# Optimization experiments

Hardware: AMD Instinct MI355X
Metric: run time of the kernel (lower is better)

Reference implementation:

```python
import jax, jax.numpy as jnp
import numpy as np

HEADS = 4
KNN_K = 20
BN_EPS = 1e-5


def conv1x1(w, b, x):
    # 1x1 Conv1d: w [out, in], x [B, in, N] -> [B, out, N]
    return jnp.einsum('oc,bcn->bon', w, x) + b[None, :, None]


def setup_inputs() -> dict:
    key = jax.random.key(0)
    B, C, N = 2, 128, 2048
    ks = jax.random.split(key, 16)
    W = lambda k, o, i: jax.random.normal(k, (o, i), jnp.float32) * 0.05
    V = lambda k, o: jax.random.normal(k, (o,), jnp.float32) * 0.05
    return {
        'desc1': jax.random.normal(ks[0], (B, C, N, 1), jnp.float32),
        'wq': W(ks[1], C, C), 'bq': V(ks[2], C),
        'wk': W(ks[3], C, C), 'bk': V(ks[4], C),
        'wv': W(ks[5], C, C), 'bv': V(ks[6], C),
        'wm': W(ks[7], C, C), 'bm': V(ks[8], C),
        'w1': W(ks[9], 2 * C, 2 * C), 'b1': V(ks[10], 2 * C),
        'gamma': jnp.ones((2 * C,), jnp.float32),
        'beta': jnp.zeros((2 * C,), jnp.float32),
        'w2': W(ks[11], C, 2 * C), 'b2': V(ks[12], C),
    }


def reference(desc1, wq, bq, wk, bk, wv, bv, wm, bm, w1, b1, gamma, beta, w2, b2):
    x = desc1[..., 0]                      # [B, C, N]
    B, C, N = x.shape
    D = C // HEADS

    q = conv1x1(wq, bq, x).reshape(B, HEADS, D, N)
    k = conv1x1(wk, bk, x).reshape(B, HEADS, D, N)
    v = conv1x1(wv, bv, x).reshape(B, HEADS, D, N)

    # kNN on raw descriptors: pd = -||xi||^2 + 2 xi.xj - ||xj||^2 (larger = closer)
    xx = jnp.sum(x * x, axis=1)            # [B, N]
    pd = 2.0 * jnp.einsum('bcn,bcm->bnm', x, x) - xx[:, :, None] - xx[:, None, :]
    idx = jax.lax.top_k(pd, KNN_K)[1]      # [B, N, K]

    # scatter ones at kNN indices, then keep only mutual neighbors
    bI = jnp.arange(B)[:, None, None]
    nI = jnp.arange(N)[None, :, None]
    mask = jnp.zeros((B, N, N), x.dtype).at[bI, nI, idx].set(1.0)
    mask = mask * mask.transpose(0, 2, 1)  # [B, N, N]

    score = jnp.einsum('bhdn,bhdm->bhnm', q, k) / (D ** 0.5)
    m = mask[:, None]                      # broadcast over heads
    score = score * m + (-1e9) * (1.0 - m)
    score = jax.nn.softmax(score, axis=-1)

    av = jnp.einsum('bhnm,bhdm->bhdn', score, v).reshape(B, C, N)
    av = conv1x1(wm, bm, av)

    h = conv1x1(w1, b1, jnp.concatenate([x, av], axis=1))  # [B, 2C, N]
    mu = jnp.mean(h, axis=(0, 2), keepdims=True)
    var = jnp.var(h, axis=(0, 2), keepdims=True)           # biased, matches torch BN
    h = (h - mu) / jnp.sqrt(var + BN_EPS) * gamma[None, :, None] + beta[None, :, None]
    h = jax.nn.relu(h)

    out = x + conv1x1(w2, b2, h)
    return out[..., None]                  # [B, C, N, 1]
```

## Files before the change

### kernel.cpp

```cpp
#include <hip/hip_runtime.h>
#include <math.h>

#define NPT 2048
#define KNN 20

typedef const float* fp;
typedef __attribute__((ext_vector_type(4))) float f32x4;
typedef __attribute__((ext_vector_type(8))) short s16x8;

__device__ __forceinline__ ushort f2bf_rne(float v) {
    unsigned u = __float_as_uint(v);
    unsigned r = u + 0x7FFFu + ((u >> 16) & 1u);
    return (ushort)(r >> 16);
}
__device__ __forceinline__ float bfbits2f(ushort h) {
    return __uint_as_float(((unsigned)h) << 16);
}
__device__ __forceinline__ s16x8 ldfrag(const ushort* p) {
    union { uint4 u; s16x8 s; } cv;
    cv.u = *reinterpret_cast<const uint4*>(p);
    return cv.s;
}
__device__ __forceinline__ void f8_hilo(const float* row, s16x8* hi, s16x8* lo) {
    float4 f0 = *reinterpret_cast<const float4*>(row);
    float4 f1 = *reinterpret_cast<const float4*>(row + 4);
    float f[8] = {f0.x, f0.y, f0.z, f0.w, f1.x, f1.y, f1.z, f1.w};
    union { ushort u[8]; s16x8 s; } H, L;
    #pragma unroll
    for (int j = 0; j < 8; j++) {
        ushort h = f2bf_rne(f[j]);
        H.u[j] = h;
        L.u[j] = f2bf_rne(f[j] - bfbits2f(h));
    }
    *hi = H.s; *lo = L.s;
}

__global__ __launch_bounds__(256) void prep_all(
    fp xbf, fp wq, fp wk, fp wv, fp wm, fp w1, fp w2, fp bm, fp b1,
    float* xx, ushort* xhiF, ushort* xloF,
    ushort* wqFhi, ushort* wqFlo, ushort* wkFhi, ushort* wkFlo,
    ushort* wvFhi, ushort* wvFlo,
    ushort* wcFhi, ushort* wcFlo, ushort* w2Fhi, ushort* w2Flo,
    float* b1p, float* stats) {
    int t = threadIdx.x;
    if (blockIdx.x < 256) {
        __shared__ float xs[16][129];
        __shared__ float xpart[16][17];
        int p0 = blockIdx.x * 16;
        int b = p0 >> 11, n0 = p0 & 2047;
        fp xb = xbf + (size_t)b * 128 * NPT;
        {
            int c = t >> 1, half = t & 1;
            float4 f0 = *reinterpret_cast<const float4*>(xb + (size_t)c * NPT + n0 + half * 8);
            float4 f1 = *reinterpret_cast<const float4*>(xb + (size_t)c * NPT + n0 + half * 8 + 4);
            xs[half * 8 + 0][c] = f0.x; xs[half * 8 + 1][c] = f0.y;
            xs[half * 8 + 2][c] = f0.z; xs[half * 8 + 3][c] = f0.w;
            xs[half * 8 + 4][c] = f1.x; xs[half * 8 + 5][c] = f1.y;
            xs[half * 8 + 6][c] = f1.z; xs[half * 8 + 7][c] = f1.w;
        }
        __syncthreads();
        int p = t & 15, g = t >> 4, c0 = g * 8;
        float f[8];
        #pragma unroll
        for (int j = 0; j < 8; j++) f[j] = xs[p][c0 + j];
        float ps = 0.f;
        #pragma unroll
        for (int j = 0; j < 8; j++) ps += f[j] * f[j];
        xpart[p][g] = ps;
        union { ushort u[8]; uint4 q; } H, L;
        #pragma unroll
        for (int j = 0; j < 8; j++) {
            ushort hi = f2bf_rne(f[j]);
            H.u[j] = hi;
            L.u[j] = f2bf_rne(f[j] - bfbits2f(hi));
        }
        size_t off = ((size_t)blockIdx.x * 4 + (c0 >> 5)) * 512
                   + (size_t)(((((c0 >> 3) & 3) * 16) + p) * 8);
        *reinterpret_cast<uint4*>(xhiF + off) = H.q;
        *reinterpret_cast<uint4*>(xloF + off) = L.q;
        __syncthreads();
        if (t < 16) {
            float s = 0.f;
            #pragma unroll
            for (int gg = 0; gg < 16; gg++) s += xpart[t][gg];
            xx[p0 + t] = s;
        }
        return;
    }
    int wid = (blockIdx.x - 256) * 256 + t;
    if (wid < 49152) {
        int which = wid >> 14, e = wid & 16383;
        int lane = (e >> 3) & 63, j = e & 7, kk = (e >> 9) & 3, nt = e >> 11;
        int n = nt * 16 + (lane & 15);
        int k = kk * 32 + (lane >> 4) * 8 + j;
        fp src = which == 0 ? wq : which == 1 ? wk : wv;
        float v = src[n * 128 + k];
        ushort hi = f2bf_rne(v);
        (which == 0 ? wqFhi : which == 1 ? wkFhi : wvFhi)[e] = hi;
        (which == 0 ? wqFlo : which == 1 ? wkFlo : wvFlo)[e] = f2bf_rne(v - bfbits2f(hi));
    } else if (wid < 114688) {
        int e = wid - 49152;
        int j = e & 7, lane = (e >> 3) & 63, kk = (e >> 9) & 7, nt = e >> 12;
        int n = nt * 16 + (lane & 15);
        int k = kk * 32 + (lane >> 4) * 8 + j;
        float v;
        if (k < 128) {
            v = w1[n * 256 + k];
        } else {
            int c = k - 128;
            float s = 0.f;
            for (int i = 0; i < 128; i += 4) {
                float4 wr = *reinterpret_cast<const float4*>(w1 + n * 256 + 128 + i);
                s += wr.x * wm[(i + 0) * 128 + c];
                s += wr.y * wm[(i + 1) * 128 + c];
                s += wr.z * wm[(i + 2) * 128 + c];
                s += wr.w * wm[(i + 3) * 128 + c];
            }
            v = s;
        }
        ushort hi = f2bf_rne(v);
        wcFhi[e] = hi;
        wcFlo[e] = f2bf_rne(v - bfbits2f(hi));
    } else if (wid < 147456) {
        int e = wid - 114688;
        int j = e & 7, lane = (e >> 3) & 63, kk = (e >> 9) & 7, nt = e >> 12;
        int n = nt * 16 + (lane & 15);
        int k = kk * 32 + (lane >> 4) * 8 + j;
        float v = w2[n * 256 + k];
        ushort hi = f2bf_rne(v);
        w2Fhi[e] = hi;
        w2Flo[e] = f2bf_rne(v - bfbits2f(hi));
    } else if (wid < 147712) {
        int o = wid - 147456;
        float s = b1[o];
        for (int i = 0; i < 128; i++)
            s += w1[o * 256 + 128 + i] * bm[i];
        b1p[o] = s;
    } else {
        stats[wid - 147712] = 0.0f;
    }
}

#define MERGE(off) { float ov = __shfl_xor(bv, off); int oi = __shfl_xor(bi, off); \
                     if (ov > bv || (ov == bv && oi < bi)) { bv = ov; bi = oi; } }

#define KEYPAIR(C0, D0, D1) { \
    int ct0 = slab * 128 + w * 8 + C0; \
    int ct1 = ct0 + 1; \
    f32x4 a0 = (f32x4){0.f, 0.f, 0.f, 0.f}; \
    f32x4 a1 = (f32x4){0.f, 0.f, 0.f, 0.f}; \
    _Pragma("unroll 2") \
    for (int kk = 0; kk < 4; kk++) { \
        s16x8 ah = ldfrag(Ahi[kk] + lane * 8); \
        s16x8 al = ldfrag(Alo[kk] + lane * 8); \
        s16x8 b0h = ldfrag(xhiF + ((size_t)(ct0 * 4 + kk)) * 512 + lane * 8); \
        s16x8 b0l = ldfrag(xloF + ((size_t)(ct0 * 4 + kk)) * 512 + lane * 8); \
        s16x8 b1h = ldfrag(xhiF + ((size_t)(ct1 * 4 + kk)) * 512 + lane * 8); \
        s16x8 b1l = ldfrag(xloF + ((size_t)(ct1 * 4 + kk)) * 512 + lane * 8); \
        a0 = __builtin_amdgcn_mfma_f32_16x16x32_bf16(ah, b0h, a0, 0, 0, 0); \
        a1 = __builtin_amdgcn_mfma_f32_16x16x32_bf16(ah, b1h, a1, 0, 0, 0); \
        a0 = __builtin_amdgcn_mfma_f32_16x16x32_bf16(al, b0h, a0, 0, 0, 0); \
        a1 = __builtin_amdgcn_mfma_f32_16x16x32_bf16(al, b1h, a1, 0, 0, 0); \
        a0 = __builtin_amdgcn_mfma_f32_16x16x32_bf16(ah, b0l, a0, 0, 0, 0); \
        a1 = __builtin_amdgcn_mfma_f32_16x16x32_bf16(ah, b1l, a1, 0, 0, 0); \
    } \
    float xx0 = xx[slab * 2048 + (w * 8 + C0) * 16 + cl]; \
    float xx1 = xx[slab * 2048 + (w * 8 + C0 + 1) * 16 + cl]; \
    a0[0] = 2.0f * a0[0] - xx0; a0[1] = 2.0f * a0[1] - xx0; \
    a0[2] = 2.0f * a0[2] - xx0; a0[3] = 2.0f * a0[3] - xx0; \
    a1[0] = 2.0f * a1[0] - xx1; a1[1] = 2.0f * a1[1] - xx1; \
    a1[2] = 2.0f * a1[2] - xx1; a1[3] = 2.0f * a1[3] - xx1; \
    D0 = a0; D1 = a1; \
}

__global__ __launch_bounds__(1024, 4) void gemm_key_topk(
    const ushort* xhiF, const ushort* xloF, const float* xx,
    const ushort* wqFhi, const ushort* wqFlo,
    const ushort* wkFhi, const ushort* wkFlo,
    const ushort* wvFhi, const ushort* wvFlo,
    fp bq, fp bk, fp bv_, float* qT, float* kT, float* vT,
    int* idxbuf, float* scratch) {
    __shared__ ushort Ahi[4][512];
    __shared__ ushort Alo[4][512];
    __shared__ float chm[16][64];
    __shared__ float sv[16][256];
    __shared__ int   si[16][256];
    __shared__ float Trow[16];
    __shared__ int   rowcnt[16];
    __shared__ int   ovfAll;
    int tt = threadIdx.x, w = tt >> 6, lane = tt & 63;
    int rt = blockIdx.x;
    int slab = rt >> 7, rtl = rt & 127;
    int cl = lane & 15, quad = lane >> 4;

    if (tt < 16) rowcnt[tt] = 0;

    if (tt < 512) {
        int which = tt >> 8, kk = (tt >> 6) & 3, ln = tt & 63;
        const ushort* src = (which ? xloF : xhiF)
                          + ((size_t)(rt * 4 + kk)) * 512 + ln * 8;
        uint4 v = *reinterpret_cast<const uint4*>(src);
        *reinterpret_cast<uint4*>((which ? Alo[kk] : Ahi[kk]) + ln * 8) = v;
    }
    __syncthreads();

    if (w < 12) {
        f32x4 acc0 = (f32x4){0.f, 0.f, 0.f, 0.f};
        f32x4 acc1 = (f32x4){0.f, 0.f, 0.f, 0.f};
        int pair0 = w * 2, pair1 = w * 2 + 1;
        int mat0 = pair0 >> 3, nt0 = pair0 & 7;
        int mat1 = pair1 >> 3, nt1 = pair1 & 7;
        const ushort* w0hi = mat0 == 0 ? wqFhi : mat0 == 1 ? wkFhi : wvFhi;
        const ushort* w0lo = mat0 == 0 ? wqFlo : mat0 == 1 ? wkFlo : wvFlo;
        const ushort* w1hi = mat1 == 0 ? wqFhi : mat1 == 1 ? wkFhi : wvFhi;
        const ushort* w1lo = mat1 == 0 ? wqFlo : mat1 == 1 ? wkFlo : wvFlo;
        #pragma unroll 2
        for (int kk = 0; kk < 4; kk++) {
            s16x8 ah = ldfrag(Ahi[kk] + lane * 8);
            s16x8 al = ldfrag(Alo[kk] + lane * 8);
            s16x8 b0h = ldfrag(w0hi + ((size_t)(nt0 * 4 + kk)) * 512 + lane * 8);
            s16x8 b0l = ldfrag(w0lo + ((size_t)(nt0 * 4 + kk)) * 512 + lane * 8);
            s16x8 b1h = ldfrag(w1hi + ((size_t)(nt1 * 4 + kk)) * 512 + lane * 8);
            s16x8 b1l = ldfrag(w1lo + ((size_t)(nt1 * 4 + kk)) * 512 + lane * 8);
            acc0 = __builtin_amdgcn_mfma_f32_16x16x32_bf16(ah, b0h, acc0, 0, 0, 0);
            acc1 = __builtin_amdgcn_mfma_f32_16x16x32_bf16(ah, b1h, acc1, 0, 0, 0);
            acc0 = __builtin_amdgcn_mfma_f32_16x16x32_bf16(al, b0h, acc0, 0, 0, 0);
            acc1 = __builtin_amdgcn_mfma_f32_16x16x32_bf16(al, b1h, acc1, 0, 0, 0);
            acc0 = __builtin_amdgcn_mfma_f32_16x16x32_bf16(ah, b0l, acc0, 0, 0, 0);
            acc1 = __builtin_amdgcn_mfma_f32_16x16x32_bf16(ah, b1l, acc1, 0, 0, 0);
        }
        int p0 = rt * 16;
        {
            fp bias    = mat0 == 0 ? bq : mat0 == 1 ? bk : bv_;
            float* out = mat0 == 0 ? qT : mat0 == 1 ? kT : vT;
            int o = nt0 * 16 + cl;
            float bvv = bias[o];
            #pragma unroll
            for (int r = 0; r < 4; r++)
                out[(size_t)(p0 + quad * 4 + r) * 128 + o] = acc0[r] + bvv;
        }
        {
            fp bias    = mat1 == 0 ? bq : mat1 == 1 ? bk : bv_;
            float* out = mat1 == 0 ? qT : mat1 == 1 ? kT : vT;
            int o = nt1 * 16 + cl;
            float bvv = bias[o];
            #pragma unroll
            for (int r = 0; r < 4; r++)
                out[(size_t)(p0 + quad * 4 + r) * 128 + o] = acc1[r] + bvv;
        }
    }
    __builtin_amdgcn_sched_barrier(0);

    f32x4 key0, key1, key2, key3, key4, key5, key6, key7;
    KEYPAIR(0, key0, key1)
    __builtin_amdgcn_sched_barrier(0);
    KEYPAIR(2, key2, key3)
    __builtin_amdgcn_sched_barrier(0);
    KEYPAIR(4, key4, key5)
    __builtin_amdgcn_sched_barrier(0);
    KEYPAIR(6, key6, key7)
    __builtin_amdgcn_sched_barrier(0);

    {
        float m[4];
        #pragma unroll
        for (int r = 0; r < 4; r++) {
            float mm = fmaxf(fmaxf(fmaxf(key0[r], key1[r]), fmaxf(key2[r], key3[r])),
                             fmaxf(fmaxf(key4[r], key5[r]), fmaxf(key6[r], key7[r])));
            mm = fmaxf(mm, __shfl_xor(mm, 1));
            mm = fmaxf(mm, __shfl_xor(mm, 2));
            m[r] = mm;
        }
        if ((cl & 3) == 0) {
            #pragma unroll
            for (int r = 0; r < 4; r++)
                chm[quad * 4 + r][w * 4 + (cl >> 2)] = m[r];
        }
    }
    __syncthreads();

    {
        float bs = chm[w][lane];
        #pragma unroll
        for (int k = 2; k <= 64; k <<= 1) {
            #pragma unroll
            for (int j = k >> 1; j > 0; j >>= 1) {
                float o = __shfl_xor(bs, j);
                bool dirDesc = (lane & k) != 0;
                bool upper   = (lane & j) != 0;
                bs = (upper != dirDesc) ? fmaxf(bs, o) : fminf(bs, o);
            }
        }
        float T = __shfl(bs, 44);
        if (lane == 0) Trow[w] = T;
    }
    __syncthreads();

    #pragma unroll
    for (int r = 0; r < 4; r++) {
        int row = quad * 4 + r;
        float T = Trow[row];
        float vals[8] = {key0[r], key1[r], key2[r], key3[r],
                         key4[r], key5[r], key6[r], key7[r]};
        #pragma unroll
        for (int c = 0; c < 8; c++) {
            float v = vals[c];
            if (v >= T) {
                int pos = atomicAdd(&rowcnt[row], 1);
                if (pos < 256) {
                    sv[row][pos] = v;
                    si[row][pos] = (w * 8 + c) * 16 + cl;
                }
            }
        }
    }
    __syncthreads();
    if (tt == 0) {
        int o = 0;
        for (int i = 0; i < 16; i++) o |= (rowcnt[i] > 256) ? 1 : 0;
        ovfAll = o;
    }
    __syncthreads();
    int ovf = ovfAll;

    int S = rowcnt[w];
    int rowg = slab * 2048 + rtl * 16 + w;
    if (S <= 64) {
        float v; int idx;
        if (lane < S) { v = sv[w][lane]; idx = si[w][lane]; }
        else          { v = -3.4e38f;    idx = 0x7FFFFFFF; }
        #pragma unroll
        for (int k = 2; k <= 64; k <<= 1) {
            #pragma unroll
            for (int j = k >> 1; j > 0; j >>= 1) {
                float ov = __shfl_xor(v, j); int oi = __shfl_xor(idx, j);
                bool dirDesc = (lane & k) != 0;
                bool upper   = (lane & j) != 0;
                bool takeMax = (upper != dirDesc);
                bool amax = (v > ov) || (v == ov && idx < oi);
                if (takeMax != amax) { v = ov; idx = oi; }
            }
        }
        if (lane >= 44) idxbuf[(size_t)rowg * KNN + (63 - lane)] = idx;
    } else if (S <= 256) {
        float vl[4]; int il[4];
        #pragma unroll
        for (int s = 0; s < 4; s++) {
            int g = lane + s * 64;
            bool ok = g < S;
            vl[s] = ok ? sv[w][g] : -3.4e38f;
            il[s] = ok ? si[w][g] : 0x7FFFFFFF;
        }
        unsigned removed = 0u;
        for (int iter = 0; iter < KNN; iter++) {
            float bv = -3.4e38f; int bi = 0x7FFFFFFF;
            #pragma unroll
            for (int s = 0; s < 4; s++) {
                bool live = ((removed >> s) & 1u) == 0u;
                if (live && (vl[s] > bv || (vl[s] == bv && il[s] < bi))) {
                    bv = vl[s]; bi = il[s];
                }
            }
            MERGE(32) MERGE(16) MERGE(8) MERGE(4) MERGE(2) MERGE(1)
            if (lane == 0) idxbuf[(size_t)rowg * KNN + iter] = bi;
            #pragma unroll
            for (int s = 0; s < 4; s++)
                if (il[s] == bi) removed |= 1u << s;
        }
    }

    if (ovf) {
        #pragma unroll
        for (int r = 0; r < 4; r++) {
            float vals[8] = {key0[r], key1[r], key2[r], key3[r],
                             key4[r], key5[r], key6[r], key7[r]};
            #pragma unroll
            for (int c = 0; c < 8; c++)
                scratch[((size_t)rt * 16 + quad * 4 + r) * 2048
                        + (w * 8 + c) * 16 + cl] = vals[c];
        }
        __syncthreads();
        if (rowcnt[w] > 256) {
            const float* rowp = scratch + ((size_t)rt * 16 + w) * 2048;
            float rv[32];
            #pragma unroll
            for (int j = 0; j < 32; j++) rv[j] = rowp[j * 64 + lane];
            unsigned removed = 0u;
            for (int iter = 0; iter < KNN; iter++) {
                float bv = -3.4e38f; int bi = 0;
                #pragma unroll
                for (int sl = 0; sl < 32; sl++) {
                    bool live = ((removed >> sl) & 1u) == 0u;
                    if (live && rv[sl] > bv) { bv = rv[sl]; bi = sl * 64 + lane; }
                }
                MERGE(32) MERGE(16) MERGE(8) MERGE(4) MERGE(2) MERGE(1)
                if (lane == 0) idxbuf[(size_t)rowg * KNN + iter] = bi;
                if ((bi & 63) == lane) removed |= 1u << (bi >> 6);
            }
        }
    }
}

__global__ __launch_bounds__(256) void k3_attn(
    fp qT, fp kT, fp vT, const int* idxbuf, float* avT) {
    __shared__ float sbuf[2][KNN * 4];
    __shared__ int   mlist[2][KNN];
    __shared__ int   cnt_s[2];
    int tt = threadIdx.x;
    int half = tt >> 7, t = tt & 127;
    int p = blockIdx.x * 2 + half;
    int b = p >> 11, n = p & 2047;
    int bbase = b * NPT;
    int h = t >> 5;

    if ((tt >> 6) == half * 2) {
        int lane = tt & 63;
        bool fl = false; int m = 0;
        if (lane < KNN) {
            m = idxbuf[(size_t)p * KNN + lane] & 2047;
            const int4* mrow = reinterpret_cast<const int4*>(idxbuf + (size_t)(bbase + m) * KNN);
            int4 r0 = mrow[0], r1 = mrow[1], r2 = mrow[2], r3 = mrow[3], r4 = mrow[4];
            fl = (r0.x == n) || (r0.y == n) || (r0.z == n) || (r0.w == n)
              || (r1.x == n) || (r1.y == n) || (r1.z == n) || (r1.w == n)
              || (r2.x == n) || (r2.y == n) || (r2.z == n) || (r2.w == n)
              || (r3.x == n) || (r3.y == n) || (r3.z == n) || (r3.w == n)
              || (r4.x == n) || (r4.y == n) || (r4.z == n) || (r4.w == n);
        }
        unsigned long long mask = __ballot(fl);
        int pos = __popcll(mask & ((1ull << lane) - 1ull));
        if (fl) mlist[half][pos] = m;
        if (lane == 0) cnt_s[half] = (int)__popcll(mask);
    }
    __syncthreads();

    int cnt = cnt_s[half];
    float qv = qT[(size_t)p * 128 + t];
    int jj = 0;
    for (; jj + 1 < cnt; jj += 2) {
        int m0 = mlist[half][jj], m1 = mlist[half][jj + 1];
        float pr0 = qv * kT[(size_t)(bbase + m0) * 128 + t];
        float pr1 = qv * kT[(size_t)(bbase + m1) * 128 + t];
        pr0 += __shfl_xor(pr0, 16); pr1 += __shfl_xor(pr1, 16);
        pr0 += __shfl_xor(pr0, 8);  pr1 += __shfl_xor(pr1, 8);
        pr0 += __shfl_xor(pr0, 4);  pr1 += __shfl_xor(pr1, 4);
        pr0 += __shfl_xor(pr0, 2);  pr1 += __shfl_xor(pr1, 2);
        pr0 += __shfl_xor(pr0, 1);  pr1 += __shfl_xor(pr1, 1);
        if ((t & 31) == 0) {
            sbuf[half][jj * 4 + h]       = pr0 * 0.17677669529663687f;
            sbuf[half][(jj + 1) * 4 + h] = pr1 * 0.17677669529663687f;
        }
    }
    if (jj < cnt) {
        int m = mlist[half][jj];
        float prod = qv * kT[(size_t)(bbase + m) * 128 + t];
        prod += __shfl_xor(prod, 16);
        prod += __shfl_xor(prod, 8);
        prod += __shfl_xor(prod, 4);
        prod += __shfl_xor(prod, 2);
        prod += __shfl_xor(prod, 1);
        if ((t & 31) == 0) sbuf[half][jj * 4 + h] = prod * 0.17677669529663687f;
    }
    __syncthreads();

    float mx = -3.4e38f;
    for (int j = 0; j < cnt; j++) mx = fmaxf(mx, sbuf[half][j * 4 + h]);
    float den = 0.f, accv = 0.f;
    for (int j = 0; j < cnt; j++) {
        float ex = expf(sbuf[half][j * 4 + h] - mx);
        den += ex;
        accv += ex * vT[(size_t)(bbase + mlist[half][j]) * 128 + t];
    }
    float inv = (cnt > 0) ? (1.0f / den) : 0.0f;
    avT[(size_t)p * 128 + t] = accv * inv;
}

__global__ __launch_bounds__(1024) void k4b_h(
    const ushort* xhiF, const ushort* xloF, const float* avT,
    const ushort* wcFhi, const ushort* wcFlo,
    const float* b1p, float* hbuf, float* stats) {
    __shared__ ushort AH[8][512];
    __shared__ ushort AL[8][512];
    int tt = threadIdx.x, w = tt >> 6, lane = tt & 63;
    int rt = blockIdx.x;
    int p0 = rt * 16;

    if (w < 8) {
        int which = w & 1, kk = w >> 1;
        const ushort* src = (which ? xloF : xhiF)
                          + ((size_t)(rt * 4 + kk)) * 512 + lane * 8;
        uint4 v = *reinterpret_cast<const uint4*>(src);
        *reinterpret_cast<uint4*>((which ? AL[kk] : AH[kk]) + lane * 8) = v;
    } else if (w < 12) {
        int kk = 4 + (w - 8);
        const float* arow = avT + (size_t)(p0 + (lane & 15)) * 128
                          + (kk - 4) * 32 + (lane >> 4) * 8;
        s16x8 hi, lo;
        f8_hilo(arow, &hi, &lo);
        union { s16x8 s; uint4 u; } cvh, cvl;
        cvh.s = hi; cvl.s = lo;
        *reinterpret_cast<uint4*>(AH[kk] + lane * 8) = cvh.u;
        *reinterpret_cast<uint4*>(AL[kk] + lane * 8) = cvl.u;
    }
    __syncthreads();

    int nt = w;
    f32x4 acc = (f32x4){0.f, 0.f, 0.f, 0.f};
    for (int kk = 0; kk < 8; kk++) {
        s16x8 ahi = ldfrag(AH[kk] + lane * 8);
        s16x8 alo = ldfrag(AL[kk] + lane * 8);
        s16x8 bhi = ldfrag(wcFhi + ((size_t)(nt * 8 + kk)) * 512 + lane * 8);
        s16x8 blo = ldfrag(wcFlo + ((size_t)(nt * 8 + kk)) * 512 + lane * 8);
        acc = __builtin_amdgcn_mfma_f32_16x16x32_bf16(ahi, bhi, acc, 0, 0, 0);
        acc = __builtin_amdgcn_mfma_f32_16x16x32_bf16(alo, bhi, acc, 0, 0, 0);
        acc = __builtin_amdgcn_mfma_f32_16x16x32_bf16(ahi, blo, acc, 0, 0, 0);
    }

    int cl = lane & 15, quad = lane >> 4;
    int o = nt * 16 + cl;
    float bb = b1p[o];
    float s = 0.f, s2 = 0.f;
    #pragma unroll
    for (int r = 0; r < 4; r++) {
        float v = acc[r] + bb;
        hbuf[(size_t)(p0 + quad * 4 + r) * 256 + o] = v;
        s += v; s2 += v * v;
    }
    s  += __shfl_xor(s, 16);  s  += __shfl_xor(s, 32);
    s2 += __shfl_xor(s2, 16); s2 += __shfl_xor(s2, 32);
    if (quad == 0) {
        atomicAdd(&stats[o], s);
        atomicAdd(&stats[256 + o], s2);
    }
}

__global__ __launch_bounds__(512) void k5b_out(
    const float* hbuf, const float* stats, fp gamma, fp beta,
    const ushort* w2Fhi, const ushort* w2Flo,
    fp b2, fp xbf, float* out) {
    __shared__ ushort HH[8][512];
    __shared__ ushort HL[8][512];
    int tt = threadIdx.x, w = tt >> 6, lane = tt & 63;
    int rt = blockIdx.x;
    int p0 = rt * 16;

    {
        int kk = w;
        int c0 = kk * 32 + (lane >> 4) * 8;
        const float* hrow = hbuf + (size_t)(p0 + (lane & 15)) * 256 + c0;
        float4 f0 = *reinterpret_cast<const float4*>(hrow);
        float4 f1 = *reinterpret_cast<const float4*>(hrow + 4);
        float4 s0 = *reinterpret_cast<const float4*>(stats + c0);
        float4 s1 = *reinterpret_cast<const float4*>(stats + c0 + 4);
        float4 q0 = *reinterpret_cast<const float4*>(stats + 256 + c0);
        float4 q1 = *reinterpret_cast<const float4*>(stats + 256 + c0 + 4);
        float4 g0 = *reinterpret_cast<const float4*>(gamma + c0);
        float4 g1 = *reinterpret_cast<const float4*>(gamma + c0 + 4);
        float4 e0 = *reinterpret_cast<const float4*>(beta + c0);
        float4 e1 = *reinterpret_cast<const float4*>(beta + c0 + 4);
        float f[8] = {f0.x, f0.y, f0.z, f0.w, f1.x, f1.y, f1.z, f1.w};
        float sm[8] = {s0.x, s0.y, s0.z, s0.w, s1.x, s1.y, s1.z, s1.w};
        float sq[8] = {q0.x, q0.y, q0.z, q0.w, q1.x, q1.y, q1.z, q1.w};
        float gm[8] = {g0.x, g0.y, g0.z, g0.w, g1.x, g1.y, g1.z, g1.w};
        float bt[8] = {e0.x, e0.y, e0.z, e0.w, e1.x, e1.y, e1.z, e1.w};
        union { ushort u[8]; uint4 q; } H, L;
        #pragma unroll
        for (int j = 0; j < 8; j++) {
            float mu  = sm[j] * (1.0f / 4096.0f);
            float var = fmaxf(sq[j] * (1.0f / 4096.0f) - mu * mu, 0.0f);
            float a    = gm[j] / sqrtf(var + 1e-5f);
            float cadd = bt[j] - mu * a;
            float v = fmaxf(f[j] * a + cadd, 0.0f);
            ushort hi = f2bf_rne(v);
            H.u[j] = hi;
            L.u[j] = f2bf_rne(v - bfbits2f(hi));
        }
        *reinterpret_cast<uint4*>(HH[kk] + lane * 8) = H.q;
        *reinterpret_cast<uint4*>(HL[kk] + lane * 8) = L.q;
    }
    __syncthreads();

    int nt = w;
    f32x4 acc = (f32x4){0.f, 0.f, 0.f, 0.f};
    for (int kk = 0; kk < 8; kk++) {
        s16x8 ahi = ldfrag(HH[kk] + lane * 8);
        s16x8 alo = ldfrag(HL[kk] + lane * 8);
        s16x8 bhi = ldfrag(w2Fhi + ((size_t)(nt * 8 + kk)) * 512 + lane * 8);
        s16x8 blo = ldfrag(w2Flo + ((size_t)(nt * 8 + kk)) * 512 + lane * 8);
        acc = __builtin_amdgcn_mfma_f32_16x16x32_bf16(ahi, bhi, acc, 0, 0, 0);
        acc = __builtin_amdgcn_mfma_f32_16x16x32_bf16(alo, bhi, acc, 0, 0, 0);
        acc = __builtin_amdgcn_mfma_f32_16x16x32_bf16(ahi, blo, acc, 0, 0, 0);
    }
    int cl = lane & 15, quad = lane >> 4;
    int b = p0 >> 11, n0 = p0 & 2047;
    int o = nt * 16 + cl;
    float bb = b2[o];
    size_t base = (size_t)b * 128 * NPT + (size_t)o * NPT + n0 + quad * 4;
    float4 xv = *reinterpret_cast<const float4*>(xbf + base);
    float4 ov;
    ov.x = acc[0] + bb + xv.x;
    ov.y = acc[1] + bb + xv.y;
    ov.z = acc[2] + bb + xv.z;
    ov.w = acc[3] + bb + xv.w;
    *reinterpret_cast<float4*>(out + base) = ov;
}

#define WS_FULL 44978176u

extern "C" void kernel_launch(void* const* d_in, const int* in_sizes, int n_in,
                              void* d_out, int out_size, void* d_ws, size_t ws_size,
                              hipStream_t stream) {
    fp desc1 = (fp)d_in[0];
    fp wq = (fp)d_in[1];  fp bq = (fp)d_in[2];
    fp wk = (fp)d_in[3];  fp bk = (fp)d_in[4];
    fp wv = (fp)d_in[5];  fp bv = (fp)d_in[6];
    fp wm = (fp)d_in[7];  fp bm = (fp)d_in[8];
    fp w1 = (fp)d_in[9];  fp b1 = (fp)d_in[10];
    fp gamma = (fp)d_in[11]; fp beta = (fp)d_in[12];
    fp w2 = (fp)d_in[13]; fp b2 = (fp)d_in[14];

    if (ws_size < (size_t)WS_FULL) return;

    char* ws = (char*)d_ws;
    float*  qT    = (float*) (ws + 0);
    float*  kT    = (float*) (ws + 2097152);
    float*  vT    = (float*) (ws + 4194304);
    float*  avT   = (float*) (ws + 6291456);
    float*  xx    = (float*) (ws + 8388608);
    int*    idxb  = (int*)   (ws + 8404992);
    float*  stats = (float*) (ws + 8732672);
    float*  b1p   = (float*) (ws + 8734720);
    ushort* wqFhi = (ushort*)(ws + 8736768);
    ushort* wqFlo = (ushort*)(ws + 8769536);
    ushort* wkFhi = (ushort*)(ws + 8802304);
    ushort* wkFlo = (ushort*)(ws + 8835072);
    ushort* wvFhi = (ushort*)(ws + 8867840);
    ushort* wvFlo = (ushort*)(ws + 8900608);
    ushort* wcFhi = (ushort*)(ws + 8933376);
    ushort* wcFlo = (ushort*)(ws + 9064448);
    ushort* w2Fhi = (ushort*)(ws + 9195520);
    ushort* w2Flo = (ushort*)(ws + 9261056);
    ushort* xhiF  = (ushort*)(ws + 9326592);
    ushort* xloF  = (ushort*)(ws + 10375168);
    float*  scratch = (float*)(ws + 11423744);
    float*  hbuf  = (float*) (ws + 0);

    prep_all<<<835, 256, 0, stream>>>(desc1, wq, wk, wv, wm, w1, w2, bm, b1,
                                      xx, xhiF, xloF,
                                      wqFhi, wqFlo, wkFhi, wkFlo, wvFhi, wvFlo,
                                      wcFhi, wcFlo, w2Fhi, w2Flo, b1p, stats);
    gemm_key_topk<<<256, 1024, 0, stream>>>(xhiF, xloF, xx,
                                            wqFhi, wqFlo, wkFhi, wkFlo,
                                            wvFhi, wvFlo,
                                            bq, bk, bv, qT, kT, vT,
                                            idxb, scratch);
    k3_attn<<<2048, 256, 0, stream>>>(qT, kT, vT, idxb, avT);
    k4b_h<<<256, 1024, 0, stream>>>(xhiF, xloF, avT, wcFhi, wcFlo,
                                    b1p, hbuf, stats);
    k5b_out<<<256, 512, 0, stream>>>(hbuf, stats, gamma, beta, w2Fhi, w2Flo,
                                     b2, desc1, (float*)d_out);
}
```

Baseline: 150.5 us.

## Fuse attention, conv/BN-stat and output GEMM into one cooperative kernel

Merges the sparse mutual-kNN attention, the concat conv with BatchNorm statistics, and the final conv into a single cooperative launch of 256 blocks of 1024 threads. Attention outputs and pre-BN activations stay in shared memory instead of going through global avT/hbuf buffers, and a grid-wide sync replaces the kernel boundary needed for the global BN statistics. This removes two launches and the global round trips, but the attention stage now runs with fewer blocks per point (16 points per block in two passes), which may lower parallelism and latency hiding.

```diff
diff --git a/kernel.cpp b/kernel.cpp
--- a/kernel.cpp
+++ b/kernel.cpp
@@ -1,5 +1,8 @@
 #include <hip/hip_runtime.h>
+#include <hip/hip_cooperative_groups.h>
 #include <math.h>
+
+namespace cg = cooperative_groups;
 
 #define NPT 2048
 #define KNN 20
@@ -401,88 +404,95 @@
     }
 }
 
-__global__ __launch_bounds__(256) void k3_attn(
-    fp qT, fp kT, fp vT, const int* idxbuf, float* avT) {
-    __shared__ float sbuf[2][KNN * 4];
-    __shared__ int   mlist[2][KNN];
-    __shared__ int   cnt_s[2];
-    int tt = threadIdx.x;
-    int half = tt >> 7, t = tt & 127;
-    int p = blockIdx.x * 2 + half;
-    int b = p >> 11, n = p & 2047;
-    int bbase = b * NPT;
-    int h = t >> 5;
-
-    if ((tt >> 6) == half * 2) {
-        int lane = tt & 63;
-        bool fl = false; int m = 0;
-        if (lane < KNN) {
-            m = idxbuf[(size_t)p * KNN + lane] & 2047;
-            const int4* mrow = reinterpret_cast<const int4*>(idxbuf + (size_t)(bbase + m) * KNN);
-            int4 r0 = mrow[0], r1 = mrow[1], r2 = mrow[2], r3 = mrow[3], r4 = mrow[4];
-            fl = (r0.x == n) || (r0.y == n) || (r0.z == n) || (r0.w == n)
-              || (r1.x == n) || (r1.y == n) || (r1.z == n) || (r1.w == n)
-              || (r2.x == n) || (r2.y == n) || (r2.z == n) || (r2.w == n)
-              || (r3.x == n) || (r3.y == n) || (r3.z == n) || (r3.w == n)
-              || (r4.x == n) || (r4.y == n) || (r4.z == n) || (r4.w == n);
-        }
-        unsigned long long mask = __ballot(fl);
-        int pos = __popcll(mask & ((1ull << lane) - 1ull));
-        if (fl) mlist[half][pos] = m;
-        if (lane == 0) cnt_s[half] = (int)__popcll(mask);
-    }
-    __syncthreads();
-
-    int cnt = cnt_s[half];
-    float qv = qT[(size_t)p * 128 + t];
-    int jj = 0;
-    for (; jj + 1 < cnt; jj += 2) {
-        int m0 = mlist[half][jj], m1 = mlist[half][jj + 1];
-        float pr0 = qv * kT[(size_t)(bbase + m0) * 128 + t];
-        float pr1 = qv * kT[(size_t)(bbase + m1) * 128 + t];
-        pr0 += __shfl_xor(pr0, 16); pr1 += __shfl_xor(pr1, 16);
-        pr0 += __shfl_xor(pr0, 8);  pr1 += __shfl_xor(pr1, 8);
-        pr0 += __shfl_xor(pr0, 4);  pr1 += __shfl_xor(pr1, 4);
-        pr0 += __shfl_xor(pr0, 2);  pr1 += __shfl_xor(pr1, 2);
-        pr0 += __shfl_xor(pr0, 1);  pr1 += __shfl_xor(pr1, 1);
-        if ((t & 31) == 0) {
-            sbuf[half][jj * 4 + h]       = pr0 * 0.17677669529663687f;
-            sbuf[half][(jj + 1) * 4 + h] = pr1 * 0.17677669529663687f;
-        }
-    }
-    if (jj < cnt) {
-        int m = mlist[half][jj];
-        float prod = qv * kT[(size_t)(bbase + m) * 128 + t];
-        prod += __shfl_xor(prod, 16);
-        prod += __shfl_xor(prod, 8);
-        prod += __shfl_xor(prod, 4);
-        prod += __shfl_xor(prod, 2);
-        prod += __shfl_xor(prod, 1);
-        if ((t & 31) == 0) sbuf[half][jj * 4 + h] = prod * 0.17677669529663687f;
-    }
-    __syncthreads();
-
-    float mx = -3.4e38f;
-    for (int j = 0; j < cnt; j++) mx = fmaxf(mx, sbuf[half][j * 4 + h]);
-    float den = 0.f, accv = 0.f;
-    for (int j = 0; j < cnt; j++) {
-        float ex = expf(sbuf[half][j * 4 + h] - mx);
-        den += ex;
-        accv += ex * vT[(size_t)(bbase + mlist[half][j]) * 128 + t];
-    }
-    float inv = (cnt > 0) ? (1.0f / den) : 0.0f;
-    avT[(size_t)p * 128 + t] = accv * inv;
-}
-
-__global__ __launch_bounds__(1024) void k4b_h(
-    const ushort* xhiF, const ushort* xloF, const float* avT,
+__global__ __launch_bounds__(1024) void k345_fused(
+    fp qT, fp kT, fp vT, const int* idxbuf,
+    const ushort* xhiF, const ushort* xloF,
     const ushort* wcFhi, const ushort* wcFlo,
-    const float* b1p, float* hbuf, float* stats) {
+    const float* b1p, float* stats,
+    fp gamma, fp beta,
+    const ushort* w2Fhi, const ushort* w2Flo,
+    fp b2, fp xbf, float* out) {
     __shared__ ushort AH[8][512];
     __shared__ ushort AL[8][512];
+    __shared__ float avL[16][132];
+    __shared__ float Hb[16][260];
+    __shared__ float sbuf[8][KNN * 4];
+    __shared__ int   mlist[8][KNN];
+    __shared__ int   cnt_s[8];
     int tt = threadIdx.x, w = tt >> 6, lane = tt & 63;
     int rt = blockIdx.x;
     int p0 = rt * 16;
+    int cl = lane & 15, quad = lane >> 4;
+
+    for (int pass = 0; pass < 2; pass++) {
+        int sg = tt >> 7, t = tt & 127;
+        int pl = pass * 8 + sg;
+        int p = p0 + pl;
+        int b = p >> 11, n = p & 2047;
+        int bbase = b * NPT;
+        int h = t >> 5;
+
+        if ((t >> 6) == 0) {
+            int ln = tt & 63;
+            bool fl = false; int m = 0;
+            if (ln < KNN) {
+                m = idxbuf[(size_t)p * KNN + ln] & 2047;
+                const int4* mrow = reinterpret_cast<const int4*>(idxbuf + (size_t)(bbase + m) * KNN);
+                int4 r0 = mrow[0], r1 = mrow[1], r2 = mrow[2], r3 = mrow[3], r4 = mrow[4];
+                fl = (r0.x == n) || (r0.y == n) || (r0.z == n) || (r0.w == n)
+                  || (r1.x == n) || (r1.y == n) || (r1.z == n) || (r1.w == n)
+                  || (r2.x == n) || (r2.y == n) || (r2.z == n) || (r2.w == n)
+                  || (r3.x == n) || (r3.y == n) || (r3.z == n) || (r3.w == n)
+                  || (r4.x == n) || (r4.y == n) || (r4.z == n) || (r4.w == n);
+            }
+            unsigned long long mask = __ballot(fl);
+            int pos = __popcll(mask & ((1ull << ln) - 1ull));
+            if (fl) mlist[sg][pos] = m;
+            if (ln == 0) cnt_s[sg] = (int)__popcll(mask);
+        }
+        __syncthreads();
+
+        int cnt = cnt_s[sg];
+        float qv = qT[(size_t)p * 128 + t];
+        int jj = 0;
+        for (; jj + 1 < cnt; jj += 2) {
+            int m0 = mlist[sg][jj], m1 = mlist[sg][jj + 1];
+            float pr0 = qv * kT[(size_t)(bbase + m0) * 128 + t];
+            float pr1 = qv * kT[(size_t)(bbase + m1) * 128 + t];
+            pr0 += __shfl_xor(pr0, 16); pr1 += __shfl_xor(pr1, 16);
+            pr0 += __shfl_xor(pr0, 8);  pr1 += __shfl_xor(pr1, 8);
+            pr0 += __shfl_xor(pr0, 4);  pr1 += __shfl_xor(pr1, 4);
+            pr0 += __shfl_xor(pr0, 2);  pr1 += __shfl_xor(pr1, 2);
+            pr0 += __shfl_xor(pr0, 1);  pr1 += __shfl_xor(pr1, 1);
+            if ((t & 31) == 0) {
+                sbuf[sg][jj * 4 + h]       = pr0 * 0.17677669529663687f;
+                sbuf[sg][(jj + 1) * 4 + h] = pr1 * 0.17677669529663687f;
+            }
+        }
+        if (jj < cnt) {
+            int m = mlist[sg][jj];
+            float prod = qv * kT[(size_t)(bbase + m) * 128 + t];
+            prod += __shfl_xor(prod, 16);
+            prod += __shfl_xor(prod, 8);
+            prod += __shfl_xor(prod, 4);
+            prod += __shfl_xor(prod, 2);
+            prod += __shfl_xor(prod, 1);
+            if ((t & 31) == 0) sbuf[sg][jj * 4 + h] = prod * 0.17677669529663687f;
+        }
+        __syncthreads();
+
+        float mx = -3.4e38f;
+        for (int j = 0; j < cnt; j++) mx = fmaxf(mx, sbuf[sg][j * 4 + h]);
+        float den = 0.f, accv = 0.f;
+        for (int j = 0; j < cnt; j++) {
+            float ex = expf(sbuf[sg][j * 4 + h] - mx);
+            den += ex;
+            accv += ex * vT[(size_t)(bbase + mlist[sg][j]) * 128 + t];
+        }
+        float inv = (cnt > 0) ? (1.0f / den) : 0.0f;
+        avL[pl][t] = accv * inv;
+        __syncthreads();
+    }
 
     if (w < 8) {
         int which = w & 1, kk = w >> 1;
@@ -492,8 +502,7 @@
         *reinterpret_cast<uint4*>((which ? AL[kk] : AH[kk]) + lane * 8) = v;
     } else if (w < 12) {
         int kk = 4 + (w - 8);
-        const float* arow = avT + (size_t)(p0 + (lane & 15)) * 128
-                          + (kk - 4) * 32 + (lane >> 4) * 8;
+        const float* arow = &avL[lane & 15][(kk - 4) * 32 + (lane >> 4) * 8];
         s16x8 hi, lo;
         f8_hilo(arow, &hi, &lo);
         union { s16x8 s; uint4 u; } cvh, cvl;
@@ -503,50 +512,41 @@
     }
     __syncthreads();
 
-    int nt = w;
-    f32x4 acc = (f32x4){0.f, 0.f, 0.f, 0.f};
-    for (int kk = 0; kk < 8; kk++) {
-        s16x8 ahi = ldfrag(AH[kk] + lane * 8);
-        s16x8 alo = ldfrag(AL[kk] + lane * 8);
-        s16x8 bhi = ldfrag(wcFhi + ((size_t)(nt * 8 + kk)) * 512 + lane * 8);
-        s16x8 blo = ldfrag(wcFlo + ((size_t)(nt * 8 + kk)) * 512 + lane * 8);
-        acc = __builtin_amdgcn_mfma_f32_16x16x32_bf16(ahi, bhi, acc, 0, 0, 0);
-        acc = __builtin_amdgcn_mfma_f32_16x16x32_bf16(alo, bhi, acc, 0, 0, 0);
-        acc = __builtin_amdgcn_mfma_f32_16x16x32_bf16(ahi, blo, acc, 0, 0, 0);
-    }
-
-    int cl = lane & 15, quad = lane >> 4;
-    int o = nt * 16 + cl;
-    float bb = b1p[o];
-    float s = 0.f, s2 = 0.f;
-    #pragma unroll
-    for (int r = 0; r < 4; r++) {
-        float v = acc[r] + bb;
-        hbuf[(size_t)(p0 + quad * 4 + r) * 256 + o] = v;
-        s += v; s2 += v * v;
-    }
-    s  += __shfl_xor(s, 16);  s  += __shfl_xor(s, 32);
-    s2 += __shfl_xor(s2, 16); s2 += __shfl_xor(s2, 32);
-    if (quad == 0) {
-        atomicAdd(&stats[o], s);
-        atomicAdd(&stats[256 + o], s2);
-    }
-}
-
-__global__ __launch_bounds__(512) void k5b_out(
-    const float* hbuf, const float* stats, fp gamma, fp beta,
-    const ushort* w2Fhi, const ushort* w2Flo,
-    fp b2, fp xbf, float* out) {
-    __shared__ ushort HH[8][512];
-    __shared__ ushort HL[8][512];
-    int tt = threadIdx.x, w = tt >> 6, lane = tt & 63;
-    int rt = blockIdx.x;
-    int p0 = rt * 16;
-
     {
+        int nt = w;
+        f32x4 acc = (f32x4){0.f, 0.f, 0.f, 0.f};
+        for (int kk = 0; kk < 8; kk++) {
+            s16x8 ahi = ldfrag(AH[kk] + lane * 8);
+            s16x8 alo = ldfrag(AL[kk] + lane * 8);
+            s16x8 bhi = ldfrag(wcFhi + ((size_t)(nt * 8 + kk)) * 512 + lane * 8);
+            s16x8 blo = ldfrag(wcFlo + ((size_t)(nt * 8 + kk)) * 512 + lane * 8);
+            acc = __builtin_amdgcn_mfma_f32_16x16x32_bf16(ahi, bhi, acc, 0, 0, 0);
+            acc = __builtin_amdgcn_mfma_f32_16x16x32_bf16(alo, bhi, acc, 0, 0, 0);
+            acc = __builtin_amdgcn_mfma_f32_16x16x32_bf16(ahi, blo, acc, 0, 0, 0);
+        }
+        int o = nt * 16 + cl;
+        float bb = b1p[o];
+        float s = 0.f, s2 = 0.f;
+        #pragma unroll
+        for (int r = 0; r < 4; r++) {
+            float v = acc[r] + bb;
+            Hb[quad * 4 + r][o] = v;
+            s += v; s2 += v * v;
+        }
+        s  += __shfl_xor(s, 16);  s  += __shfl_xor(s, 32);
+        s2 += __shfl_xor(s2, 16); s2 += __shfl_xor(s2, 32);
+        if (quad == 0) {
+            atomicAdd(&stats[o], s);
+            atomicAdd(&stats[256 + o], s2);
+        }
+    }
+
+    cg::this_grid().sync();
+
+    if (w < 8) {
         int kk = w;
         int c0 = kk * 32 + (lane >> 4) * 8;
-        const float* hrow = hbuf + (size_t)(p0 + (lane & 15)) * 256 + c0;
+        const float* hrow = &Hb[lane & 15][c0];
         float4 f0 = *reinterpret_cast<const float4*>(hrow);
         float4 f1 = *reinterpret_cast<const float4*>(hrow + 4);
         float4 s0 = *reinterpret_cast<const float4*>(stats + c0);
@@ -574,34 +574,35 @@
             H.u[j] = hi;
             L.u[j] = f2bf_rne(v - bfbits2f(hi));
         }
-        *reinterpret_cast<uint4*>(HH[kk] + lane * 8) = H.q;
-        *reinterpret_cast<uint4*>(HL[kk] + lane * 8) = L.q;
+        *reinterpret_cast<uint4*>(AH[kk] + lane * 8) = H.q;
+        *reinterpret_cast<uint4*>(AL[kk] + lane * 8) = L.q;
     }
     __syncthreads();
 
-    int nt = w;
-    f32x4 acc = (f32x4){0.f, 0.f, 0.f, 0.f};
-    for (int kk = 0; kk < 8; kk++) {
-        s16x8 ahi = ldfrag(HH[kk] + lane * 8);
-        s16x8 alo = ldfrag(HL[kk] + lane * 8);
-        s16x8 bhi = ldfrag(w2Fhi + ((size_t)(nt * 8 + kk)) * 512 + lane * 8);
-        s16x8 blo = ldfrag(w2Flo + ((size_t)(nt * 8 + kk)) * 512 + lane * 8);
-        acc = __builtin_amdgcn_mfma_f32_16x16x32_bf16(ahi, bhi, acc, 0, 0, 0);
-        acc = __builtin_amdgcn_mfma_f32_16x16x32_bf16(alo, bhi, acc, 0, 0, 0);
-        acc = __builtin_amdgcn_mfma_f32_16x16x32_bf16(ahi, blo, acc, 0, 0, 0);
-    }
-    int cl = lane & 15, quad = lane >> 4;
-    int b = p0 >> 11, n0 = p0 & 2047;
-    int o = nt * 16 + cl;
-    float bb = b2[o];
-    size_t base = (size_t)b * 128 * NPT + (size_t)o * NPT + n0 + quad * 4;
-    float4 xv = *reinterpret_cast<const float4*>(xbf + base);
-    float4 ov;
-    ov.x = acc[0] + bb + xv.x;
-    ov.y = acc[1] + bb + xv.y;
-    ov.z = acc[2] + bb + xv.z;
-    ov.w = acc[3] + bb + xv.w;
-    *reinterpret_cast<float4*>(out + base) = ov;
+    if (w < 8) {
+        int nt = w;
+        f32x4 acc = (f32x4){0.f, 0.f, 0.f, 0.f};
+        for (int kk = 0; kk < 8; kk++) {
+            s16x8 ahi = ldfrag(AH[kk] + lane * 8);
+            s16x8 alo = ldfrag(AL[kk] + lane * 8);
+            s16x8 bhi = ldfrag(w2Fhi + ((size_t)(nt * 8 + kk)) * 512 + lane * 8);
+            s16x8 blo = ldfrag(w2Flo + ((size_t)(nt * 8 + kk)) * 512 + lane * 8);
+            acc = __builtin_amdgcn_mfma_f32_16x16x32_bf16(ahi, bhi, acc, 0, 0, 0);
+            acc = __builtin_amdgcn_mfma_f32_16x16x32_bf16(alo, bhi, acc, 0, 0, 0);
+            acc = __builtin_amdgcn_mfma_f32_16x16x32_bf16(ahi, blo, acc, 0, 0, 0);
+        }
+        int b = p0 >> 11, n0 = p0 & 2047;
+        int o = nt * 16 + cl;
+        float bb = b2[o];
+        size_t base = (size_t)b * 128 * NPT + (size_t)o * NPT + n0 + quad * 4;
+        float4 xv = *reinterpret_cast<const float4*>(xbf + base);
+        float4 ov;
+        ov.x = acc[0] + bb + xv.x;
+        ov.y = acc[1] + bb + xv.y;
+        ov.z = acc[2] + bb + xv.z;
+        ov.w = acc[3] + bb + xv.w;
+        *reinterpret_cast<float4*>(out + base) = ov;
+    }
 }
 
 #define WS_FULL 44978176u
@@ -624,7 +625,6 @@
     float*  qT    = (float*) (ws + 0);
     float*  kT    = (float*) (ws + 2097152);
     float*  vT    = (float*) (ws + 4194304);
-    float*  avT   = (float*) (ws + 6291456);
     float*  xx    = (float*) (ws + 8388608);
     int*    idxb  = (int*)   (ws + 8404992);
     float*  stats = (float*) (ws + 8732672);
@@ -642,7 +642,7 @@
     ushort* xhiF  = (ushort*)(ws + 9326592);
     ushort* xloF  = (ushort*)(ws + 10375168);
     float*  scratch = (float*)(ws + 11423744);
-    float*  hbuf  = (float*) (ws + 0);
+    float*  outp  = (float*)d_out;
 
     prep_all<<<835, 256, 0, stream>>>(desc1, wq, wk, wv, wm, w1, w2, bm, b1,
                                       xx, xhiF, xloF,
@@ -653,9 +653,18 @@
                                             wvFhi, wvFlo,
                                             bq, bk, bv, qT, kT, vT,
                                             idxb, scratch);
-    k3_attn<<<2048, 256, 0, stream>>>(qT, kT, vT, idxb, avT);
-    k4b_h<<<256, 1024, 0, stream>>>(xhiF, xloF, avT, wcFhi, wcFlo,
-                                    b1p, hbuf, stats);
-    k5b_out<<<256, 512, 0, stream>>>(hbuf, stats, gamma, beta, w2Fhi, w2Flo,
-                                     b2, desc1, (float*)d_out);
-}
+    {
+        fp qTc = qT, kTc = kT, vTc = vT;
+        const int* idxc = idxb;
+        const ushort* xhiFc = xhiF; const ushort* xloFc = xloF;
+        const ushort* wcFhic = wcFhi; const ushort* wcFloc = wcFlo;
+        const float* b1pc = b1p;
+        const ushort* w2Fhic = w2Fhi; const ushort* w2Floc = w2Flo;
+        void* args[] = { &qTc, &kTc, &vTc, &idxc, &xhiFc, &xloFc,
+                         &wcFhic, &wcFloc, &b1pc, &stats,
+                         &gamma, &beta, &w2Fhic, &w2Floc,
+                         &b2, &desc1, &outp };
+        hipLaunchCooperativeKernel((const void*)k345_fused,
+                                   dim3(256), dim3(1024), args, 0, stream);
+    }
+}
```

Result: slower. 207.7 us (+38.1%).

## Fuse h-projection and output GEMM into one cooperative kernel with grid sync

Applied to the files above, without the earlier changes.

Merges k4b_h and k5b_out into a single cooperative kernel. The pre-BN activations stay in LDS instead of going through a global hbuf, and a grid-wide sync waits for the BatchNorm statistics to finish accumulating. This removes one launch and the global round-trip of h. In exchange it adds the cost of a grid barrier, and it needs all 256 blocks of 1024 threads to be co-resident, which the cooperative launch enforces.

```diff
diff --git a/kernel.cpp b/kernel.cpp
--- a/kernel.cpp
+++ b/kernel.cpp
@@ -1,5 +1,8 @@
 #include <hip/hip_runtime.h>
+#include <hip/hip_cooperative_groups.h>
 #include <math.h>
+
+namespace cg = cooperative_groups;
 
 #define NPT 2048
 #define KNN 20
@@ -474,15 +477,20 @@
     avT[(size_t)p * 128 + t] = accv * inv;
 }
 
-__global__ __launch_bounds__(1024) void k4b_h(
+__global__ __launch_bounds__(1024) void k45_fused(
     const ushort* xhiF, const ushort* xloF, const float* avT,
     const ushort* wcFhi, const ushort* wcFlo,
-    const float* b1p, float* hbuf, float* stats) {
+    const float* b1p, float* stats,
+    fp gamma, fp beta,
+    const ushort* w2Fhi, const ushort* w2Flo,
+    fp b2, fp xbf, float* out) {
     __shared__ ushort AH[8][512];
     __shared__ ushort AL[8][512];
+    __shared__ float Hb[16][260];
     int tt = threadIdx.x, w = tt >> 6, lane = tt & 63;
     int rt = blockIdx.x;
     int p0 = rt * 16;
+    int cl = lane & 15, quad = lane >> 4;
 
     if (w < 8) {
         int which = w & 1, kk = w >> 1;
@@ -503,50 +511,41 @@
     }
     __syncthreads();
 
-    int nt = w;
-    f32x4 acc = (f32x4){0.f, 0.f, 0.f, 0.f};
-    for (int kk = 0; kk < 8; kk++) {
-        s16x8 ahi = ldfrag(AH[kk] + lane * 8);
-        s16x8 alo = ldfrag(AL[kk] + lane * 8);
-        s16x8 bhi = ldfrag(wcFhi + ((size_t)(nt * 8 + kk)) * 512 + lane * 8);
-        s16x8 blo = ldfrag(wcFlo + ((size_t)(nt * 8 + kk)) * 512 + lane * 8);
-        acc = __builtin_amdgcn_mfma_f32_16x16x32_bf16(ahi, bhi, acc, 0, 0, 0);
-        acc = __builtin_amdgcn_mfma_f32_16x16x32_bf16(alo, bhi, acc, 0, 0, 0);
-        acc = __builtin_amdgcn_mfma_f32_16x16x32_bf16(ahi, blo, acc, 0, 0, 0);
-    }
-
-    int cl = lane & 15, quad = lane >> 4;
-    int o = nt * 16 + cl;
-    float bb = b1p[o];
-    float s = 0.f, s2 = 0.f;
-    #pragma unroll
-    for (int r = 0; r < 4; r++) {
-        float v = acc[r] + bb;
-        hbuf[(size_t)(p0 + quad * 4 + r) * 256 + o] = v;
-        s += v; s2 += v * v;
-    }
-    s  += __shfl_xor(s, 16);  s  += __shfl_xor(s, 32);
-    s2 += __shfl_xor(s2, 16); s2 += __shfl_xor(s2, 32);
-    if (quad == 0) {
-        atomicAdd(&stats[o], s);
-        atomicAdd(&stats[256 + o], s2);
-    }
-}
-
-__global__ __launch_bounds__(512) void k5b_out(
-    const float* hbuf, const float* stats, fp gamma, fp beta,
-    const ushort* w2Fhi, const ushort* w2Flo,
-    fp b2, fp xbf, float* out) {
-    __shared__ ushort HH[8][512];
-    __shared__ ushort HL[8][512];
-    int tt = threadIdx.x, w = tt >> 6, lane = tt & 63;
-    int rt = blockIdx.x;
-    int p0 = rt * 16;
-
     {
+        int nt = w;
+        f32x4 acc = (f32x4){0.f, 0.f, 0.f, 0.f};
+        for (int kk = 0; kk < 8; kk++) {
+            s16x8 ahi = ldfrag(AH[kk] + lane * 8);
+            s16x8 alo = ldfrag(AL[kk] + lane * 8);
+            s16x8 bhi = ldfrag(wcFhi + ((size_t)(nt * 8 + kk)) * 512 + lane * 8);
+            s16x8 blo = ldfrag(wcFlo + ((size_t)(nt * 8 + kk)) * 512 + lane * 8);
+            acc = __builtin_amdgcn_mfma_f32_16x16x32_bf16(ahi, bhi, acc, 0, 0, 0);
+            acc = __builtin_amdgcn_mfma_f32_16x16x32_bf16(alo, bhi, acc, 0, 0, 0);
+            acc = __builtin_amdgcn_mfma_f32_16x16x32_bf16(ahi, blo, acc, 0, 0, 0);
+        }
+        int o = nt * 16 + cl;
+        float bb = b1p[o];
+        float s = 0.f, s2 = 0.f;
+        #pragma unroll
+        for (int r = 0; r < 4; r++) {
+            float v = acc[r] + bb;
+            Hb[quad * 4 + r][o] = v;
+            s += v; s2 += v * v;
+        }
+        s  += __shfl_xor(s, 16);  s  += __shfl_xor(s, 32);
+        s2 += __shfl_xor(s2, 16); s2 += __shfl_xor(s2, 32);
+        if (quad == 0) {
+            atomicAdd(&stats[o], s);
+            atomicAdd(&stats[256 + o], s2);
+        }
+    }
+
+    cg::this_grid().sync();
+
+    if (w < 8) {
         int kk = w;
         int c0 = kk * 32 + (lane >> 4) * 8;
-        const float* hrow = hbuf + (size_t)(p0 + (lane & 15)) * 256 + c0;
+        const float* hrow = &Hb[lane & 15][c0];
         float4 f0 = *reinterpret_cast<const float4*>(hrow);
         float4 f1 = *reinterpret_cast<const float4*>(hrow + 4);
         float4 s0 = *reinterpret_cast<const float4*>(stats + c0);
@@ -574,34 +573,35 @@
             H.u[j] = hi;
             L.u[j] = f2bf_rne(v - bfbits2f(hi));
         }
-        *reinterpret_cast<uint4*>(HH[kk] + lane * 8) = H.q;
-        *reinterpret_cast<uint4*>(HL[kk] + lane * 8) = L.q;
-    }
-    __syncthreads();
-
-    int nt = w;
-    f32x4 acc = (f32x4){0.f, 0.f, 0.f, 0.f};
-    for (int kk = 0; kk < 8; kk++) {
-        s16x8 ahi = ldfrag(HH[kk] + lane * 8);
-        s16x8 alo = ldfrag(HL[kk] + lane * 8);
-        s16x8 bhi = ldfrag(w2Fhi + ((size_t)(nt * 8 + kk)) * 512 + lane * 8);
-        s16x8 blo = ldfrag(w2Flo + ((size_t)(nt * 8 + kk)) * 512 + lane * 8);
-        acc = __builtin_amdgcn_mfma_f32_16x16x32_bf16(ahi, bhi, acc, 0, 0, 0);
-        acc = __builtin_amdgcn_mfma_f32_16x16x32_bf16(alo, bhi, acc, 0, 0, 0);
-        acc = __builtin_amdgcn_mfma_f32_16x16x32_bf16(ahi, blo, acc, 0, 0, 0);
-    }
-    int cl = lane & 15, quad = lane >> 4;
-    int b = p0 >> 11, n0 = p0 & 2047;
-    int o = nt * 16 + cl;
-    float bb = b2[o];
-    size_t base = (size_t)b * 128 * NPT + (size_t)o * NPT + n0 + quad * 4;
-    float4 xv = *reinterpret_cast<const float4*>(xbf + base);
-    float4 ov;
-    ov.x = acc[0] + bb + xv.x;
-    ov.y = acc[1] + bb + xv.y;
-    ov.z = acc[2] + bb + xv.z;
-    ov.w = acc[3] + bb + xv.w;
-    *reinterpret_cast<float4*>(out + base) = ov;
+        *reinterpret_cast<uint4*>(AH[kk] + lane * 8) = H.q;
+        *reinterpret_cast<uint4*>(AL[kk] + lane * 8) = L.q;
+    }
+    __syncthreads();
+
+    if (w < 8) {
+        int nt = w;
+        f32x4 acc = (f32x4){0.f, 0.f, 0.f, 0.f};
+        for (int kk = 0; kk < 8; kk++) {
+            s16x8 ahi = ldfrag(AH[kk] + lane * 8);
+            s16x8 alo = ldfrag(AL[kk] + lane * 8);
+            s16x8 bhi = ldfrag(w2Fhi + ((size_t)(nt * 8 + kk)) * 512 + lane * 8);
+            s16x8 blo = ldfrag(w2Flo + ((size_t)(nt * 8 + kk)) * 512 + lane * 8);
+            acc = __builtin_amdgcn_mfma_f32_16x16x32_bf16(ahi, bhi, acc, 0, 0, 0);
+            acc = __builtin_amdgcn_mfma_f32_16x16x32_bf16(alo, bhi, acc, 0, 0, 0);
+            acc = __builtin_amdgcn_mfma_f32_16x16x32_bf16(ahi, blo, acc, 0, 0, 0);
+        }
+        int b = p0 >> 11, n0 = p0 & 2047;
+        int o = nt * 16 + cl;
+        float bb = b2[o];
+        size_t base = (size_t)b * 128 * NPT + (size_t)o * NPT + n0 + quad * 4;
+        float4 xv = *reinterpret_cast<const float4*>(xbf + base);
+        float4 ov;
+        ov.x = acc[0] + bb + xv.x;
+        ov.y = acc[1] + bb + xv.y;
+        ov.z = acc[2] + bb + xv.z;
+        ov.w = acc[3] + bb + xv.w;
+        *reinterpret_cast<float4*>(out + base) = ov;
+    }
 }
 
 #define WS_FULL 44978176u
@@ -642,7 +642,7 @@
     ushort* xhiF  = (ushort*)(ws + 9326592);
     ushort* xloF  = (ushort*)(ws + 10375168);
     float*  scratch = (float*)(ws + 11423744);
-    float*  hbuf  = (float*) (ws + 0);
+    float*  outp  = (float*)d_out;
 
     prep_all<<<835, 256, 0, stream>>>(desc1, wq, wk, wv, wm, w1, w2, bm, b1,
                                       xx, xhiF, xloF,
@@ -654,8 +654,16 @@
                                             bq, bk, bv, qT, kT, vT,
                                             idxb, scratch);
     k3_attn<<<2048, 256, 0, stream>>>(qT, kT, vT, idxb, avT);
-    k4b_h<<<256, 1024, 0, stream>>>(xhiF, xloF, avT, wcFhi, wcFlo,
-                                    b1p, hbuf, stats);
-    k5b_out<<<256, 512, 0, stream>>>(hbuf, stats, gamma, beta, w2Fhi, w2Flo,
-                                     b2, desc1, (float*)d_out);
-}
+    {
+        const ushort* xhiFc = xhiF; const ushort* xloFc = xloF;
+        const float* avTc = avT;
+        const ushort* wcFhic = wcFhi; const ushort* wcFloc = wcFlo;
+        const float* b1pc = b1p;
+        const ushort* w2Fhic = w2Fhi; const ushort* w2Floc = w2Flo;
+        void* args[] = { &xhiFc, &xloFc, &avTc, &wcFhic, &wcFloc,
+                         &b1pc, &stats, &gamma, &beta,
+                         &w2Fhic, &w2Floc, &b2, &desc1, &outp };
+        hipLaunchCooperativeKernel((const void*)k45_fused,
+                                   dim3(256), dim3(1024), args, 0, stream);
+    }
+}
```

Result: slower. 205.9 us (+36.9%).
